# Performance work log

Hardware: AMD Instinct MI355X
Metric: run time of the kernel (lower is better)

## Reference

```python
import jax, jax.numpy as jnp
import numpy as np

N_NODES = 100000
N_EDGES = 3200000


def gcn_conv(x, edge_index, W, b, num_nodes):
    # PyG GCNConv: linear transform, add self-loops, symmetric degree norm, scatter-add, bias
    h = x @ W  # [N, out]
    src = jnp.concatenate([edge_index[0], jnp.arange(num_nodes)])  # self-loops
    dst = jnp.concatenate([edge_index[1], jnp.arange(num_nodes)])
    deg = jax.ops.segment_sum(jnp.ones_like(dst, dtype=h.dtype), dst, num_segments=num_nodes)
    dinv = jnp.where(deg > 0, jax.lax.rsqrt(deg), 0.0)
    norm = dinv[src] * dinv[dst]  # [E+N]
    msg = h[src] * norm[:, None]  # gather + scale
    out = jax.ops.segment_sum(msg, dst, num_segments=num_nodes)  # scatter-add
    return out + b


def setup_inputs() -> dict:
    key = jax.random.key(0)
    k1, k2, k3, k4 = jax.random.split(key, 4)
    x = jax.random.normal(k1, (N_NODES, 18), dtype=jnp.float32)
    edge_index = jax.random.randint(k2, (2, N_EDGES), 0, N_NODES, dtype=jnp.int64)
    W1 = jax.random.normal(k3, (18, 64), dtype=jnp.float32) * (1.0 / np.sqrt(18))
    b1 = jnp.zeros((64,), dtype=jnp.float32)
    W2 = jax.random.normal(k4, (64, 32), dtype=jnp.float32) * (1.0 / np.sqrt(64))
    b2 = jnp.zeros((32,), dtype=jnp.float32)
    return {"x": x, "edge_index": edge_index, "W1": W1, "b1": b1, "W2": W2, "b2": b2}


def reference(x, edge_index, W1, b1, W2, b2):
    h = jax.nn.relu(gcn_conv(x, edge_index, W1, b1, N_NODES))
    return gcn_conv(h, edge_index, W2, b2, N_NODES)
```

## Files before the change

### kernel.cpp

```cpp
#include <hip/hip_runtime.h>

#define F0 18
#define F1 64
#define F2 32
#define BSHIFT 8
#define BNODES (1 << BSHIFT)
#define CHUNK 8192
#define CAP 9216

__global__ __launch_bounds__(256) void scatter32_kernel(const int* __restrict__ ei,
                                                        int* __restrict__ bcur,
                                                        unsigned int* __restrict__ stage,
                                                        int E, int NB) {
    __shared__ int lh[512];
    __shared__ int lb[512];
    for (int i = threadIdx.x; i < NB; i += 256) lh[i] = 0;
    __syncthreads();
    int e0 = blockIdx.x * CHUNK, e1 = min(e0 + CHUNK, E);
    for (int e = e0 + threadIdx.x; e < e1; e += 256)
        atomicAdd(&lh[ei[E + e] >> BSHIFT], 1);
    __syncthreads();
    for (int i = threadIdx.x; i < NB; i += 256) {
        int c = lh[i];
        lb[i] = c ? (i * CAP + atomicAdd(&bcur[i], c)) : 0;
        lh[i] = 0;
    }
    __syncthreads();
    for (int e = e0 + threadIdx.x; e < e1; e += 256) {
        int s = ei[e], d = ei[E + e];
        int b = d >> BSHIFT;
        int p = lb[b] + atomicAdd(&lh[b], 1);
        if (p < (b + 1) * CAP)
            stage[p] = ((unsigned)(d & (BNODES - 1)) << 24) | (unsigned)s;
    }
}

__global__ __launch_bounds__(256) void bucketfill_kernel(const unsigned int* __restrict__ stage,
                                                         const int* __restrict__ bcur,
                                                         int* __restrict__ rps,
                                                         int* __restrict__ rpe,
                                                         float* __restrict__ dinv,
                                                         int* __restrict__ csr, int n) {
    __shared__ int lcnt[BNODES];
    __shared__ int lofs[BNODES];
    int b = blockIdx.x;
    int base = b << BSHIFT;
    int nn = min(BNODES, n - base);
    int ecnt = min(bcur[b], CAP);
    int estart = b * CAP;
    int t = threadIdx.x;

    lcnt[t] = 0;
    __syncthreads();
    for (int e = estart + t; e < estart + ecnt; e += 256)
        atomicAdd(&lcnt[stage[e] >> 24], 1);
    __syncthreads();

    int v = (t < nn) ? lcnt[t] : 0;
    lofs[t] = v;
    __syncthreads();
    for (int off = 1; off < BNODES; off <<= 1) {
        int x = (t >= off) ? lofs[t - off] : 0;
        __syncthreads();
        lofs[t] += x;
        __syncthreads();
    }
    if (t < nn) {
        rps[base + t] = estart + lofs[t] - v;
        rpe[base + t] = estart + lofs[t];
        dinv[base + t] = rsqrtf((float)(v + 1));
    }
    __syncthreads();

    lcnt[t] = lofs[t] - v;
    __syncthreads();
    for (int e = estart + t; e < estart + ecnt; e += 256) {
        unsigned int pk = stage[e];
        int d = pk >> 24;
        int pos = atomicAdd(&lcnt[d], 1);
        csr[estart + pos] = (int)(pk & 0xffffffu);
    }
}


__global__ __launch_bounds__(256) void pad_kernel(const float* __restrict__ x,
                                                  const float* __restrict__ dinv,
                                                  float* __restrict__ xp, int n) {
    int gid = blockIdx.x * 256 + threadIdx.x;
    int v = gid >> 5, j = gid & 31;
    if (v >= n) return;
    xp[gid] = (j < F0) ? dinv[v] * x[v * F0 + j] : 0.f;
}

__global__ __launch_bounds__(256) void agg32_kernel(const float* __restrict__ tab,
                                                    const int* __restrict__ csr,
                                                    const int* __restrict__ rps,
                                                    const int* __restrict__ rpe,
                                                    const float* __restrict__ dinv,
                                                    const float* __restrict__ bias,
                                                    float* __restrict__ outp, int n) {
    int wid = (blockIdx.x * 256 + threadIdx.x) >> 6;
    int lane = threadIdx.x & 63;
    if (wid >= n) return;
    int sub = lane >> 3;
    int qf  = (lane & 7) << 2;
    int beg = rps[wid], end = rpe[wid];
    float4 acc = make_float4(0.f, 0.f, 0.f, 0.f);
    if (sub == 0) acc = *(const float4*)&tab[(size_t)wid * 32 + qf];
    int e = beg + sub;
    for (; e + 8 < end; e += 16) {
        int s0 = csr[e], s1 = csr[e + 8];
        float4 v0 = *(const float4*)&tab[(size_t)s0 * 32 + qf];
        float4 v1 = *(const float4*)&tab[(size_t)s1 * 32 + qf];
        acc.x += v0.x + v1.x; acc.y += v0.y + v1.y;
        acc.z += v0.z + v1.z; acc.w += v0.w + v1.w;
    }
    for (; e < end; e += 8) {
        int s = csr[e];
        float4 vv = *(const float4*)&tab[(size_t)s * 32 + qf];
        acc.x += vv.x; acc.y += vv.y; acc.z += vv.z; acc.w += vv.w;
    }
    for (int off = 8; off < 64; off <<= 1) {
        acc.x += __shfl_xor(acc.x, off, 64);
        acc.y += __shfl_xor(acc.y, off, 64);
        acc.z += __shfl_xor(acc.z, off, 64);
        acc.w += __shfl_xor(acc.w, off, 64);
    }
    if (sub == 0) {
        float dv = dinv[wid];
        float4 r;
        if (bias) {
            r.x = acc.x * dv + bias[qf];
            r.y = acc.y * dv + bias[qf + 1];
            r.z = acc.z * dv + bias[qf + 2];
            r.w = acc.w * dv + bias[qf + 3];
        } else {
            r.x = acc.x * dv; r.y = acc.y * dv; r.z = acc.z * dv; r.w = acc.w * dv;
        }
        *(float4*)&outp[(size_t)wid * 32 + qf] = r;
    }
}

__global__ __launch_bounds__(256) void gemm_fused_kernel(const float* __restrict__ ax,
                                                         const float* __restrict__ W1,
                                                         const float* __restrict__ b1,
                                                         const float* __restrict__ W2,
                                                         const float* __restrict__ dinv,
                                                         float* __restrict__ h2p, int n) {
    __shared__ float W1s[F0 * F1];
    __shared__ float W2s[F1 * F2];
    __shared__ float hid[8][F1];
    __shared__ float axs[8][32];
    int t = threadIdx.x;
    for (int i = t; i < F0 * F1; i += 256) W1s[i] = W1[i];
    for (int i = t; i < F1 * F2; i += 256) W2s[i] = W2[i];
    int lv = t >> 5, j = t & 31;
    int v = blockIdx.x * 8 + lv;
    if (v < n) axs[lv][j] = ax[(size_t)v * 32 + j];
    __syncthreads();
    float h0 = b1[j], h1 = b1[j + 32];
#pragma unroll
    for (int k = 0; k < F0; ++k) {
        float a = axs[lv][k];
        h0 += a * W1s[k * F1 + j];
        h1 += a * W1s[k * F1 + j + 32];
    }
    hid[lv][j] = fmaxf(h0, 0.f);
    hid[lv][j + 32] = fmaxf(h1, 0.f);
    __syncthreads();
    float acc = 0.f;
#pragma unroll
    for (int k = 0; k < F1; ++k) acc += hid[lv][k] * W2s[k * F2 + j];
    if (v < n) h2p[(size_t)v * 32 + j] = acc * dinv[v];
}


extern "C" void kernel_launch(void* const* d_in, const int* in_sizes, int n_in,
                              void* d_out, int out_size, void* d_ws, size_t ws_size,
                              hipStream_t stream) {
    const float* x  = (const float*)d_in[0];
    const int*   ei = (const int*)d_in[1];
    const float* W1 = (const float*)d_in[2];
    const float* b1 = (const float*)d_in[3];
    const float* W2 = (const float*)d_in[4];
    const float* b2 = (const float*)d_in[5];
    float* out = (float*)d_out;

    int n = in_sizes[0] / F0;
    int E = in_sizes[1] / 2;
    int NB = (n + BNODES - 1) >> BSHIFT;

    char* ws = (char*)d_ws;
    size_t o = 0;
    auto alloc = [&](size_t bytes) {
        char* p = ws + o;
        o = (o + bytes + 255) & ~(size_t)255;
        return p;
    };
    int*   rps   = (int*)alloc((size_t)n * 4);
    int*   rpe   = (int*)alloc((size_t)n * 4);
    float* dinv  = (float*)alloc((size_t)n * 4);
    int*   bcur  = (int*)alloc(512 * 4);
    int*   csr   = (int*)alloc((size_t)NB * CAP * 4);
    unsigned int* stage = (unsigned int*)alloc((size_t)NB * CAP * 4);
    float* ax    = (float*)alloc((size_t)n * 32 * 4);
    float* xp    = (float*)stage;
    float* h2p   = (float*)stage;
    (void)ws_size; (void)n_in; (void)out_size;

    int nchunks = (E + CHUNK - 1) / CHUNK;

    hipMemsetAsync(bcur, 0, 512 * 4, stream);
    scatter32_kernel<<<nchunks, 256, 0, stream>>>(ei, bcur, stage, E, NB);
    bucketfill_kernel<<<NB, 256, 0, stream>>>(stage, bcur, rps, rpe, dinv, csr, n);

    pad_kernel<<<(n * 32 + 255) / 256, 256, 0, stream>>>(x, dinv, xp, n);
    agg32_kernel<<<(n + 3) / 4, 256, 0, stream>>>(xp, csr, rps, rpe, dinv, nullptr, ax, n);
    gemm_fused_kernel<<<(n + 7) / 8, 256, 0, stream>>>(ax, W1, b1, W2, dinv, h2p, n);
    agg32_kernel<<<(n + 3) / 4, 256, 0, stream>>>(h2p, csr, rps, rpe, dinv, b2, out, n);
}
```

Measured before the change: 237.9 us.

## Store gather tables in fp16, sort chunk in LDS, fuse padding into bucketfill

The gathered feature tables (padded input and layer-2 pre-aggregation) are stored as fp16, which halves the bytes each random edge gather reads, while accumulation stays in fp32. The scatter kernel now sorts each edge chunk by bucket in shared memory before writing it out, so global stage writes become contiguous runs instead of scattered atomics-driven stores. The separate pad kernel is fused into bucketfill, which removes one launch and a pass over the features. fp16 storage lowers the precision of the messages.

```diff
diff --git a/kernel.cpp b/kernel.cpp
--- a/kernel.cpp
+++ b/kernel.cpp
@@ -1,37 +1,70 @@
 #include <hip/hip_runtime.h>
+#include <hip/hip_fp16.h>
 
 #define F0 18
 #define F1 64
 #define F2 32
 #define BSHIFT 8
-#define BNODES (1 << BSHIFT)
+#define BNODES 256
 #define CHUNK 8192
 #define CAP 9216
 
-__global__ __launch_bounds__(256) void scatter32_kernel(const int* __restrict__ ei,
-                                                        int* __restrict__ bcur,
-                                                        unsigned int* __restrict__ stage,
-                                                        int E, int NB) {
+__global__ __launch_bounds__(256) void scatter_sort_kernel(const int* __restrict__ ei,
+                                                           int* __restrict__ bcur,
+                                                           unsigned int* __restrict__ stage,
+                                                           int E, int NB) {
+    __shared__ unsigned int sbuf[CHUNK];
     __shared__ int lh[512];
+    __shared__ int lofs[512];
     __shared__ int lb[512];
-    for (int i = threadIdx.x; i < NB; i += 256) lh[i] = 0;
-    __syncthreads();
+    __shared__ int tmp[256];
+    int t = threadIdx.x;
     int e0 = blockIdx.x * CHUNK, e1 = min(e0 + CHUNK, E);
-    for (int e = e0 + threadIdx.x; e < e1; e += 256)
+    int ec = e1 - e0;
+
+    lh[t] = 0; lh[t + 256] = 0;
+    __syncthreads();
+    for (int e = e0 + t; e < e1; e += 256)
         atomicAdd(&lh[ei[E + e] >> BSHIFT], 1);
     __syncthreads();
-    for (int i = threadIdx.x; i < NB; i += 256) {
-        int c = lh[i];
-        lb[i] = c ? (i * CAP + atomicAdd(&bcur[i], c)) : 0;
-        lh[i] = 0;
-    }
-    __syncthreads();
-    for (int e = e0 + threadIdx.x; e < e1; e += 256) {
-        int s = ei[e], d = ei[E + e];
+
+    int c0 = lh[2 * t], c1 = lh[2 * t + 1];
+    int s = c0 + c1;
+    tmp[t] = s;
+    __syncthreads();
+    for (int off = 1; off < 256; off <<= 1) {
+        int xv = (t >= off) ? tmp[t - off] : 0;
+        __syncthreads();
+        tmp[t] += xv;
+        __syncthreads();
+    }
+    int ep = tmp[t] - s;
+    lofs[2 * t] = ep;
+    lofs[2 * t + 1] = ep + c0;
+    if (2 * t < NB && c0 > 0) lb[2 * t] = 2 * t * CAP + atomicAdd(&bcur[2 * t], c0);
+    if (2 * t + 1 < NB && c1 > 0) lb[2 * t + 1] = (2 * t + 1) * CAP + atomicAdd(&bcur[2 * t + 1], c1);
+    lh[2 * t] = 0; lh[2 * t + 1] = 0;
+    __syncthreads();
+
+    for (int e = e0 + t; e < e1; e += 256) {
+        int sN = ei[e], d = ei[E + e];
         int b = d >> BSHIFT;
-        int p = lb[b] + atomicAdd(&lh[b], 1);
-        if (p < (b + 1) * CAP)
-            stage[p] = ((unsigned)(d & (BNODES - 1)) << 24) | (unsigned)s;
+        int pos = lofs[b] + atomicAdd(&lh[b], 1);
+        sbuf[pos] = ((unsigned)(d & 255) << 24) | (unsigned)sN;
+    }
+    __syncthreads();
+
+    int b;
+    {
+        int lo = 0, hi = NB;
+        while (lo + 1 < hi) { int mid = (lo + hi) >> 1; if (lofs[mid] <= t) lo = mid; else hi = mid; }
+        b = lo;
+    }
+    for (int i = t; i < ec; i += 256) {
+        while (i >= lofs[b + 1]) ++b;
+        int g = lb[b] + (i - lofs[b]);
+        if (g < (b + 1) * CAP)
+            stage[g] = sbuf[i];
     }
 }
 
@@ -40,7 +73,9 @@
                                                          int* __restrict__ rps,
                                                          int* __restrict__ rpe,
                                                          float* __restrict__ dinv,
-                                                         int* __restrict__ csr, int n) {
+                                                         int* __restrict__ csr,
+                                                         const float* __restrict__ x,
+                                                         __half* __restrict__ xp, int n) {
     __shared__ int lcnt[BNODES];
     __shared__ int lofs[BNODES];
     int b = blockIdx.x;
@@ -60,65 +95,73 @@
     lofs[t] = v;
     __syncthreads();
     for (int off = 1; off < BNODES; off <<= 1) {
-        int x = (t >= off) ? lofs[t - off] : 0;
-        __syncthreads();
-        lofs[t] += x;
-        __syncthreads();
-    }
+        int xv = (t >= off) ? lofs[t - off] : 0;
+        __syncthreads();
+        lofs[t] += xv;
+        __syncthreads();
+    }
+    float dv = rsqrtf((float)(v + 1));
     if (t < nn) {
         rps[base + t] = estart + lofs[t] - v;
         rpe[base + t] = estart + lofs[t];
-        dinv[base + t] = rsqrtf((float)(v + 1));
-    }
-    __syncthreads();
-
-    lcnt[t] = lofs[t] - v;
-    __syncthreads();
+        dinv[base + t] = dv;
+    }
+    __syncthreads();
+    int cur0 = lofs[t] - v;
+    __syncthreads();
+    lcnt[t] = cur0;
+    ((float*)lofs)[t] = dv;
+    __syncthreads();
+
     for (int e = estart + t; e < estart + ecnt; e += 256) {
         unsigned int pk = stage[e];
         int d = pk >> 24;
         int pos = atomicAdd(&lcnt[d], 1);
         csr[estart + pos] = (int)(pk & 0xffffffu);
     }
-}
-
-
-__global__ __launch_bounds__(256) void pad_kernel(const float* __restrict__ x,
-                                                  const float* __restrict__ dinv,
-                                                  float* __restrict__ xp, int n) {
-    int gid = blockIdx.x * 256 + threadIdx.x;
-    int v = gid >> 5, j = gid & 31;
-    if (v >= n) return;
-    xp[gid] = (j < F0) ? dinv[v] * x[v * F0 + j] : 0.f;
-}
-
-__global__ __launch_bounds__(256) void agg32_kernel(const float* __restrict__ tab,
-                                                    const int* __restrict__ csr,
-                                                    const int* __restrict__ rps,
-                                                    const int* __restrict__ rpe,
-                                                    const float* __restrict__ dinv,
-                                                    const float* __restrict__ bias,
-                                                    float* __restrict__ outp, int n) {
+    for (int idx = t; idx < nn * 32; idx += 256) {
+        int lv = idx >> 5, j = idx & 31;
+        float val = (j < F0) ? ((float*)lofs)[lv] * x[(size_t)(base + lv) * F0 + j] : 0.f;
+        xp[(size_t)(base + lv) * 32 + j] = __float2half(val);
+    }
+}
+
+struct __align__(8) h4v { __half2 a, b; };
+
+__global__ __launch_bounds__(256) void agg32h_kernel(const __half* __restrict__ tab,
+                                                     const int* __restrict__ csr,
+                                                     const int* __restrict__ rps,
+                                                     const int* __restrict__ rpe,
+                                                     const float* __restrict__ dinv,
+                                                     const float* __restrict__ bias,
+                                                     float* __restrict__ outp, int n) {
     int wid = (blockIdx.x * 256 + threadIdx.x) >> 6;
     int lane = threadIdx.x & 63;
     if (wid >= n) return;
     int sub = lane >> 3;
-    int qf  = (lane & 7) << 2;
+    int q = (lane & 7) << 2;
     int beg = rps[wid], end = rpe[wid];
     float4 acc = make_float4(0.f, 0.f, 0.f, 0.f);
-    if (sub == 0) acc = *(const float4*)&tab[(size_t)wid * 32 + qf];
+    if (sub == 0) {
+        h4v sv = *(const h4v*)&tab[(size_t)wid * 32 + q];
+        float2 f0 = __half22float2(sv.a), f1 = __half22float2(sv.b);
+        acc.x = f0.x; acc.y = f0.y; acc.z = f1.x; acc.w = f1.y;
+    }
     int e = beg + sub;
     for (; e + 8 < end; e += 16) {
         int s0 = csr[e], s1 = csr[e + 8];
-        float4 v0 = *(const float4*)&tab[(size_t)s0 * 32 + qf];
-        float4 v1 = *(const float4*)&tab[(size_t)s1 * 32 + qf];
-        acc.x += v0.x + v1.x; acc.y += v0.y + v1.y;
-        acc.z += v0.z + v1.z; acc.w += v0.w + v1.w;
+        h4v v0 = *(const h4v*)&tab[(size_t)s0 * 32 + q];
+        h4v v1 = *(const h4v*)&tab[(size_t)s1 * 32 + q];
+        float2 a0 = __half22float2(v0.a), b0 = __half22float2(v0.b);
+        float2 a1 = __half22float2(v1.a), b1 = __half22float2(v1.b);
+        acc.x += a0.x + a1.x; acc.y += a0.y + a1.y;
+        acc.z += b0.x + b1.x; acc.w += b0.y + b1.y;
     }
     for (; e < end; e += 8) {
-        int s = csr[e];
-        float4 vv = *(const float4*)&tab[(size_t)s * 32 + qf];
-        acc.x += vv.x; acc.y += vv.y; acc.z += vv.z; acc.w += vv.w;
+        int s0 = csr[e];
+        h4v v0 = *(const h4v*)&tab[(size_t)s0 * 32 + q];
+        float2 a0 = __half22float2(v0.a), b0 = __half22float2(v0.b);
+        acc.x += a0.x; acc.y += a0.y; acc.z += b0.x; acc.w += b0.y;
     }
     for (int off = 8; off < 64; off <<= 1) {
         acc.x += __shfl_xor(acc.x, off, 64);
@@ -129,15 +172,9 @@
     if (sub == 0) {
         float dv = dinv[wid];
         float4 r;
-        if (bias) {
-            r.x = acc.x * dv + bias[qf];
-            r.y = acc.y * dv + bias[qf + 1];
-            r.z = acc.z * dv + bias[qf + 2];
-            r.w = acc.w * dv + bias[qf + 3];
-        } else {
-            r.x = acc.x * dv; r.y = acc.y * dv; r.z = acc.z * dv; r.w = acc.w * dv;
-        }
-        *(float4*)&outp[(size_t)wid * 32 + qf] = r;
+        r.x = acc.x * dv; r.y = acc.y * dv; r.z = acc.z * dv; r.w = acc.w * dv;
+        if (bias) { r.x += bias[q]; r.y += bias[q + 1]; r.z += bias[q + 2]; r.w += bias[q + 3]; }
+        *(float4*)&outp[(size_t)wid * 32 + q] = r;
     }
 }
 
@@ -146,7 +183,7 @@
                                                          const float* __restrict__ b1,
                                                          const float* __restrict__ W2,
                                                          const float* __restrict__ dinv,
-                                                         float* __restrict__ h2p, int n) {
+                                                         __half* __restrict__ h2p, int n) {
     __shared__ float W1s[F0 * F1];
     __shared__ float W2s[F1 * F2];
     __shared__ float hid[8][F1];
@@ -171,7 +208,7 @@
     float acc = 0.f;
 #pragma unroll
     for (int k = 0; k < F1; ++k) acc += hid[lv][k] * W2s[k * F2 + j];
-    if (v < n) h2p[(size_t)v * 32 + j] = acc * dinv[v];
+    if (v < n) h2p[(size_t)v * 32 + j] = __float2half(acc * dinv[v]);
 }
 
 
@@ -204,18 +241,17 @@
     int*   csr   = (int*)alloc((size_t)NB * CAP * 4);
     unsigned int* stage = (unsigned int*)alloc((size_t)NB * CAP * 4);
     float* ax    = (float*)alloc((size_t)n * 32 * 4);
-    float* xp    = (float*)stage;
-    float* h2p   = (float*)stage;
+    __half* xp   = (__half*)alloc((size_t)n * 32 * 2);
+    __half* h2p  = (__half*)stage;
     (void)ws_size; (void)n_in; (void)out_size;
 
     int nchunks = (E + CHUNK - 1) / CHUNK;
 
     hipMemsetAsync(bcur, 0, 512 * 4, stream);
-    scatter32_kernel<<<nchunks, 256, 0, stream>>>(ei, bcur, stage, E, NB);
-    bucketfill_kernel<<<NB, 256, 0, stream>>>(stage, bcur, rps, rpe, dinv, csr, n);
-
-    pad_kernel<<<(n * 32 + 255) / 256, 256, 0, stream>>>(x, dinv, xp, n);
-    agg32_kernel<<<(n + 3) / 4, 256, 0, stream>>>(xp, csr, rps, rpe, dinv, nullptr, ax, n);
+    scatter_sort_kernel<<<nchunks, 256, 0, stream>>>(ei, bcur, stage, E, NB);
+    bucketfill_kernel<<<NB, 256, 0, stream>>>(stage, bcur, rps, rpe, dinv, csr, x, xp, n);
+
+    agg32h_kernel<<<(n + 3) / 4, 256, 0, stream>>>(xp, csr, rps, rpe, dinv, nullptr, ax, n);
     gemm_fused_kernel<<<(n + 7) / 8, 256, 0, stream>>>(ax, W1, b1, W2, dinv, h2p, n);
-    agg32_kernel<<<(n + 3) / 4, 256, 0, stream>>>(h2p, csr, rps, rpe, dinv, b2, out, n);
-}
+    agg32h_kernel<<<(n + 3) / 4, 256, 0, stream>>>(h2p, csr, rps, rpe, dinv, b2, out, n);
+}
```

Result: no change. 242.5 us (+1.9%).
